# Kernel tuning notes

Measured on AMD Instinct MI355X. Metric: run time of the kernel, lower is better.

The kernel has to match this reference:

```python
import jax, jax.numpy as jnp
import numpy as np

N_NODES = 50000
N_EDGES = 800000
D_FEAT = 128
N_LAYERS = 3
HALF = 64  # units // 2 per kernel in tf_geometric MeanGraphSage
HIDDEN = 256
NUM_LABELS = 40


def setup_inputs() -> dict:
    key = jax.random.key(0)
    ks = jax.random.split(key, 6)
    x = jax.random.normal(ks[0], (N_NODES, D_FEAT), dtype=jnp.float32)
    edge_index = jax.random.randint(ks[1], (2, N_EDGES), 0, N_NODES, dtype=jnp.int32)
    self_kernels = jax.random.normal(ks[2], (N_LAYERS, D_FEAT, HALF), dtype=jnp.float32) * 0.05
    neighbor_kernels = jax.random.normal(ks[3], (N_LAYERS, D_FEAT, HALF), dtype=jnp.float32) * 0.05
    biases = jnp.zeros((N_LAYERS, 2 * HALF), dtype=jnp.float32)
    mlp_w1 = jax.random.normal(ks[4], (2 * HALF, HIDDEN), dtype=jnp.float32) * 0.05
    mlp_b1 = jnp.zeros((HIDDEN,), dtype=jnp.float32)
    mlp_w2 = jax.random.normal(ks[5], (HIDDEN, NUM_LABELS), dtype=jnp.float32) * 0.05
    mlp_b2 = jnp.zeros((NUM_LABELS,), dtype=jnp.float32)
    return {"x": x, "edge_index": edge_index, "self_kernels": self_kernels,
            "neighbor_kernels": neighbor_kernels, "biases": biases,
            "mlp_w1": mlp_w1, "mlp_b1": mlp_b1, "mlp_w2": mlp_w2, "mlp_b2": mlp_b2}


def reference(x, edge_index, self_kernels, neighbor_kernels, biases,
              mlp_w1, mlp_b1, mlp_w2, mlp_b2):
    n = x.shape[0]
    row, col = edge_index[0], edge_index[1]  # row: target node, col: source node
    # in-degree counts (graph is fixed across layers)
    ones = jnp.ones((edge_index.shape[1],), dtype=x.dtype)
    deg = jax.ops.segment_sum(ones, row, num_segments=n)  # [N]
    inv_deg = (1.0 / jnp.maximum(deg, 1.0))[:, None]      # [N,1]

    h = x
    for i in range(N_LAYERS):
        # mean-neighbor aggregation: gather source feats, segment-sum to targets
        nbr_sum = jax.ops.segment_sum(h[col], row, num_segments=n)  # [N,D]
        nbr_mean = nbr_sum * inv_deg
        from_self = h @ self_kernels[i]        # [N,HALF]
        from_nbr = nbr_mean @ neighbor_kernels[i]  # [N,HALF]
        h = jax.nn.relu(jnp.concatenate([from_self, from_nbr], axis=1) + biases[i])

    # MLP head (Flatten on [N,128] is a no-op)
    h = jax.nn.relu(h @ mlp_w1 + mlp_b1)
    return h @ mlp_w2 + mlp_b2
```

## Files before the change

kernel.cpp:

```cpp
#include <hip/hip_runtime.h>
#include <hip/hip_bf16.h>
#include <hip/hip_fp16.h>
#include <cstdint>
#include <cstddef>

#define N_NODES 50000
#define N_PAD   50176
#define N_EDGES 800000
#define D_FEAT  128
#define HALF    64
#define HIDDEN  256
#define LABELS  40

#define NBUCK 196
#define BCAP  5632
#define EDGES_PER_BLK 4096

#define HID_STRIDE 264

typedef __attribute__((ext_vector_type(8))) short bf16x8;
typedef __attribute__((ext_vector_type(4))) float f32x4;

#define PK_SELF(L) ((size_t)(L) * 8192)
#define PK_NBR(L)  (24576 + (size_t)(L) * 8192)
#define PK_W1      49152
#define PK_W2      81920
#define PK_TOTAL   94208

__device__ inline uint16_t f2bf_bits(float f) {
    __hip_bfloat16 b = __float2bfloat16(f);
    uint16_t u; __builtin_memcpy(&u, &b, 2); return u;
}

__device__ inline float2 h2f(uint32_t u) {
    __half2 h; __builtin_memcpy(&h, &u, 4);
    return __half22float2(h);
}

__global__ __launch_bounds__(1024) void bucket_scatter_kernel(
        const int* __restrict__ row, const int* __restrict__ col,
        int* __restrict__ bucket_cursor, uint32_t* __restrict__ staged) {
    __shared__ int hist[NBUCK];
    __shared__ int hbase[NBUCK];
    int tid  = threadIdx.x;
    int e0   = blockIdx.x * EDGES_PER_BLK;
    int eend = e0 + EDGES_PER_BLK; if (eend > N_EDGES) eend = N_EDGES;

    for (int i = tid; i < NBUCK; i += 1024) hist[i] = 0;
    __syncthreads();

    int rr[4], cc[4]; int ne = 0;
    for (int e = e0 + tid; e < eend; e += 1024) {
        rr[ne] = row[e]; cc[ne] = col[e]; ne++;
    }
    for (int i = 0; i < ne; i++) atomicAdd(&hist[rr[i] >> 8], 1);
    __syncthreads();

    for (int i = tid; i < NBUCK; i += 1024) {
        hbase[i] = atomicAdd(&bucket_cursor[i], hist[i]);
        hist[i]  = 0;
    }
    __syncthreads();

    for (int i = 0; i < ne; i++) {
        int b   = rr[i] >> 8;
        int off = atomicAdd(&hist[b], 1);
        int pos = hbase[b] + off;
        if (pos < BCAP)
            staged[(size_t)b * BCAP + pos] =
                ((uint32_t)(rr[i] & 255) << 16) | (uint32_t)cc[i];
    }
}

__global__ __launch_bounds__(1024) void bucket_fill_kernel(
        const uint32_t* __restrict__ staged, const int* __restrict__ bucket_cursor,
        int* __restrict__ deg, int* __restrict__ rowstart,
        float* __restrict__ inv_deg, int* __restrict__ csr_col) {
    __shared__ int cnt[256];
    __shared__ int excl[256];
    __shared__ int wt[4];
    __shared__ int seg[BCAP];
    __shared__ int base_s;
    int b   = blockIdx.x;
    int tid = threadIdx.x;

    if (tid < 64) {
        int partial = 0;
        for (int i = tid; i < b; i += 64) partial += bucket_cursor[i];
#pragma unroll
        for (int off = 32; off > 0; off >>= 1)
            partial += __shfl_down(partial, off, 64);
        if (tid == 0) base_s = partial;
    }
    if (tid < 256) cnt[tid] = 0;
    __syncthreads();

    int total = bucket_cursor[b]; if (total > BCAP) total = BCAP;
    int gbase = base_s;
    const uint32_t* st = staged + (size_t)b * BCAP;

    for (int i = tid; i < total; i += 1024) atomicAdd(&cnt[st[i] >> 16], 1);
    __syncthreads();

    int lane = tid & 63, wid = tid >> 6;
    int v = 0, s = 0;
    if (tid < 256) {
        v = cnt[tid]; s = v;
#pragma unroll
        for (int off = 1; off < 64; off <<= 1) {
            int t = __shfl_up(s, off, 64);
            if (lane >= off) s += t;
        }
        if (lane == 63) wt[wid] = s;
    }
    __syncthreads();
    if (tid == 0) { int a = 0; for (int i = 0; i < 4; i++) { int t = wt[i]; wt[i] = a; a += t; } }
    __syncthreads();
    if (tid < 256) {
        int ex = s - v + wt[wid];
        excl[tid] = ex;
        int node = (b << 8) + tid;
        if (node < N_NODES) {
            deg[node]      = v;
            rowstart[node] = gbase + ex;
            inv_deg[node]  = 1.0f / fmaxf((float)v, 1.0f);
        }
    }
    __syncthreads();
    for (int i = tid; i < total; i += 1024) {
        uint32_t u = st[i];
        int p = atomicAdd(&excl[u >> 16], 1);
        seg[p] = (int)(u & 0xffffu);
    }
    __syncthreads();
    for (int i = tid; i < total; i += 1024) csr_col[gbase + i] = seg[i];
}

__global__ __launch_bounds__(256) void pack_all_kernel(
        const float* __restrict__ selfk, const float* __restrict__ nbrk,
        const float* __restrict__ w1, const float* __restrict__ w2,
        __hip_bfloat16* __restrict__ wpack) {
    int m = blockIdx.y;
    const float* W; int K, Ncols, Npad; size_t dstoff;
    if (m < 3)      { W = selfk + (size_t)m*D_FEAT*HALF;      K=128; Ncols=64;  Npad=64;  dstoff = PK_SELF(m); }
    else if (m < 6) { W = nbrk  + (size_t)(m-3)*D_FEAT*HALF;  K=128; Ncols=64;  Npad=64;  dstoff = PK_NBR(m-3); }
    else if (m == 6){ W = w1;                                 K=128; Ncols=256; Npad=256; dstoff = PK_W1; }
    else            { W = w2;                                 K=256; Ncols=40;  Npad=48;  dstoff = PK_W2; }
    int ksteps = K / 32;
    int total  = ksteps * (Npad / 16) * 64;
    int t = blockIdx.x * blockDim.x + threadIdx.x;
    if (t >= total) return;
    int lane = t & 63;
    int rest = t >> 6;
    int ks   = rest % ksteps;
    int ns   = rest / ksteps;
    int colb = ns * 16 + (lane & 15);
    int kb   = ks * 32 + (lane >> 4) * 8;
    __hip_bfloat16* dst = wpack + dstoff + (size_t)t * 8;
#pragma unroll
    for (int j = 0; j < 8; j++) {
        float v = (colb < Ncols) ? W[(size_t)(kb + j) * Ncols + colb] : 0.f;
        dst[j] = __float2bfloat16(v);
    }
}

template<bool AF32>
__global__ __launch_bounds__(256, 2) void layer_gemm_kernel(
        const void* __restrict__ Ain,
        const __hip_bfloat16* __restrict__ wpack_self,
        const __hip_bfloat16* __restrict__ wpack_nbr,
        const float* __restrict__ bias,
        __hip_bfloat16* __restrict__ hout,
        uint16_t* __restrict__ zn) {
    int wave = threadIdx.x >> 6, lane = threadIdx.x & 63;
    int row0 = blockIdx.x * 128 + wave * 32;
    int lrow = lane & 15, lgrp = lane >> 4;

    const __hip_bfloat16 *hr0 = nullptr, *hr1 = nullptr;
    const float *xr0 = nullptr, *xr1 = nullptr;
    if constexpr (AF32) {
        const float* x = (const float*)Ain;
        int r0 = min(row0 + lrow, N_NODES - 1);
        int r1 = min(row0 + lrow + 16, N_NODES - 1);
        xr0 = x + (size_t)r0 * D_FEAT + lgrp * 8;
        xr1 = x + (size_t)r1 * D_FEAT + lgrp * 8;
    } else {
        const __hip_bfloat16* h = (const __hip_bfloat16*)Ain;
        hr0 = h + (size_t)(row0 + lrow) * D_FEAT + lgrp * 8;
        hr1 = hr0 + (size_t)16 * D_FEAT;
    }

    f32x4 accS[2][4] = {};
    f32x4 accN[2][4] = {};
#pragma unroll
    for (int ks = 0; ks < 4; ks++) {
        bf16x8 a0, a1;
        if constexpr (AF32) {
            float4 u0  = *(const float4*)(xr0 + ks * 32);
            float4 u0b = *(const float4*)(xr0 + ks * 32 + 4);
            float4 u1  = *(const float4*)(xr1 + ks * 32);
            float4 u1b = *(const float4*)(xr1 + ks * 32 + 4);
            float f0[8] = {u0.x, u0.y, u0.z, u0.w, u0b.x, u0b.y, u0b.z, u0b.w};
            float f1[8] = {u1.x, u1.y, u1.z, u1.w, u1b.x, u1b.y, u1b.z, u1b.w};
#pragma unroll
            for (int j = 0; j < 8; j++) { a0[j] = (short)f2bf_bits(f0[j]); a1[j] = (short)f2bf_bits(f1[j]); }
        } else {
            a0 = *(const bf16x8*)(hr0 + ks * 32);
            a1 = *(const bf16x8*)(hr1 + ks * 32);
        }
#pragma unroll
        for (int ns = 0; ns < 4; ns++) {
            bf16x8 bs = *(const bf16x8*)(wpack_self + ((size_t)(ns * 4 + ks) * 64 + lane) * 8);
            accS[0][ns] = __builtin_amdgcn_mfma_f32_16x16x32_bf16(a0, bs, accS[0][ns], 0, 0, 0);
            accS[1][ns] = __builtin_amdgcn_mfma_f32_16x16x32_bf16(a1, bs, accS[1][ns], 0, 0, 0);
            bf16x8 bn = *(const bf16x8*)(wpack_nbr + ((size_t)(ns * 4 + ks) * 64 + lane) * 8);
            accN[0][ns] = __builtin_amdgcn_mfma_f32_16x16x32_bf16(a0, bn, accN[0][ns], 0, 0, 0);
            accN[1][ns] = __builtin_amdgcn_mfma_f32_16x16x32_bf16(a1, bn, accN[1][ns], 0, 0, 0);
        }
    }
#pragma unroll
    for (int t = 0; t < 2; t++) {
#pragma unroll
        for (int ns = 0; ns < 4; ns++) {
            int colS = ns * 16 + lrow;
            float bvS = bias[colS];
#pragma unroll
            for (int i = 0; i < 4; i++) {
                int r = row0 + t * 16 + lgrp * 4 + i;
                hout[(size_t)r * D_FEAT + colS] =
                    __float2bfloat16(fmaxf(accS[t][ns][i] + bvS, 0.f));
                __half hz = __float2half(accN[t][ns][i]);
                uint16_t hb; __builtin_memcpy(&hb, &hz, 2);
                zn[(size_t)r * HALF + colS] = hb;
            }
        }
    }
}

__global__ __launch_bounds__(128) void agg8_kernel(
        const uint16_t* __restrict__ zn, const int* __restrict__ csr_col,
        const int* __restrict__ rowstart, const int* __restrict__ deg,
        const float* __restrict__ inv_deg, const float* __restrict__ bias64,
        __hip_bfloat16* __restrict__ hout) {
    int gid  = blockIdx.x * 128 + threadIdx.x;
    int wnum = gid >> 6;
    int lane = threadIdx.x & 63;
    int sub  = lane >> 3;
    int sl   = lane & 7;
    int node = wnum * 8 + sub;
    int start = rowstart[node];
    int d     = deg[node];
    const uint32_t* zw = (const uint32_t*)zn;
    float acc[8] = {};

#define ACC8H(U) { float2 t0 = h2f((U).x), t1 = h2f((U).y),            \
                   float2_dummy_##__LINE__; (void)0;                    \
    acc[0] += t0.x; acc[1] += t0.y; acc[2] += t1.x; acc[3] += t1.y;     \
    float2 t2 = h2f((U).z), t3 = h2f((U).w);                            \
    acc[4] += t2.x; acc[5] += t2.y; acc[6] += t3.x; acc[7] += t3.y; }

#undef ACC8H
#define ACC8H(U) {                                                      \
    float2 t0 = h2f((U).x); acc[0] += t0.x; acc[1] += t0.y;             \
    float2 t1 = h2f((U).y); acc[2] += t1.x; acc[3] += t1.y;             \
    float2 t2 = h2f((U).z); acc[4] += t2.x; acc[5] += t2.y;             \
    float2 t3 = h2f((U).w); acc[6] += t3.x; acc[7] += t3.y; }

    if (d > 0) {
        int last = start + d - 1;
        int s[8];
#pragma unroll
        for (int k = 0; k < 8; k++) s[k] = csr_col[min(start + k, last)];
        int j = 0;
        for (; j + 8 <= d; j += 8) {
            int p[8];
#pragma unroll
            for (int k = 0; k < 8; k++) p[k] = csr_col[min(start + j + 8 + k, last)];
            uint4 u0 = *(const uint4*)(zw + (size_t)s[0] * 32 + sl * 4);
            uint4 u1 = *(const uint4*)(zw + (size_t)s[1] * 32 + sl * 4);
            uint4 u2 = *(const uint4*)(zw + (size_t)s[2] * 32 + sl * 4);
            uint4 u3 = *(const uint4*)(zw + (size_t)s[3] * 32 + sl * 4);
            uint4 u4 = *(const uint4*)(zw + (size_t)s[4] * 32 + sl * 4);
            uint4 u5 = *(const uint4*)(zw + (size_t)s[5] * 32 + sl * 4);
            uint4 u6 = *(const uint4*)(zw + (size_t)s[6] * 32 + sl * 4);
            uint4 u7 = *(const uint4*)(zw + (size_t)s[7] * 32 + sl * 4);
            ACC8H(u0); ACC8H(u1); ACC8H(u2); ACC8H(u3);
            ACC8H(u4); ACC8H(u5); ACC8H(u6); ACC8H(u7);
#pragma unroll
            for (int k = 0; k < 8; k++) s[k] = p[k];
        }
        int r = d - j;
#pragma unroll
        for (int k = 0; k < 8; k++) {
            if (k < r) {
                uint4 u = *(const uint4*)(zw + (size_t)s[k] * 32 + sl * 4);
                ACC8H(u);
            }
        }
    }
#undef ACC8H

    float inv = inv_deg[node];
    float4 b0 = *(const float4*)(bias64 + sl * 8);
    float4 b1 = *(const float4*)(bias64 + sl * 8 + 4);
    uint4 p;
    p.x = (uint32_t)f2bf_bits(fmaxf(acc[0] * inv + b0.x, 0.f))
        | ((uint32_t)f2bf_bits(fmaxf(acc[1] * inv + b0.y, 0.f)) << 16);
    p.y = (uint32_t)f2bf_bits(fmaxf(acc[2] * inv + b0.z, 0.f))
        | ((uint32_t)f2bf_bits(fmaxf(acc[3] * inv + b0.w, 0.f)) << 16);
    p.z = (uint32_t)f2bf_bits(fmaxf(acc[4] * inv + b1.x, 0.f))
        | ((uint32_t)f2bf_bits(fmaxf(acc[5] * inv + b1.y, 0.f)) << 16);
    p.w = (uint32_t)f2bf_bits(fmaxf(acc[6] * inv + b1.z, 0.f))
        | ((uint32_t)f2bf_bits(fmaxf(acc[7] * inv + b1.w, 0.f)) << 16);
    *(uint4*)((uint32_t*)hout + (size_t)node * 64 + 32 + sl * 4) = p;
}

__global__ __launch_bounds__(256, 2) void mlp_fused_kernel(
        const __hip_bfloat16* __restrict__ h, const __hip_bfloat16* __restrict__ w1p,
        const float* __restrict__ b1, const __hip_bfloat16* __restrict__ w2p,
        const float* __restrict__ b2, float* __restrict__ out) {
    __shared__ __align__(16) uint16_t hid[128 * HID_STRIDE];
    int wave = threadIdx.x >> 6, lane = threadIdx.x & 63;
    int row0 = blockIdx.x * 128 + wave * 32;
    int lrow = lane & 15, lgrp = lane >> 4;

    {
        const __hip_bfloat16* ar0 = h + (size_t)(row0 + lrow) * D_FEAT + lgrp * 8;
        const __hip_bfloat16* ar1 = ar0 + (size_t)16 * D_FEAT;
        f32x4 acc[2][16] = {};
#pragma unroll 1
        for (int ks = 0; ks < 4; ks++) {
            bf16x8 a0 = *(const bf16x8*)(ar0 + ks * 32);
            bf16x8 a1 = *(const bf16x8*)(ar1 + ks * 32);
#pragma unroll
            for (int ns = 0; ns < 16; ns++) {
                bf16x8 bfr = *(const bf16x8*)(w1p + ((size_t)(ns * 4 + ks) * 64 + lane) * 8);
                acc[0][ns] = __builtin_amdgcn_mfma_f32_16x16x32_bf16(a0, bfr, acc[0][ns], 0, 0, 0);
                acc[1][ns] = __builtin_amdgcn_mfma_f32_16x16x32_bf16(a1, bfr, acc[1][ns], 0, 0, 0);
            }
        }
        int lbase = wave * 32;
#pragma unroll
        for (int t = 0; t < 2; t++) {
#pragma unroll
            for (int ns = 0; ns < 16; ns++) {
                int col = ns * 16 + lrow;
                float bv = b1[col];
#pragma unroll
                for (int i = 0; i < 4; i++) {
                    int lr = lbase + t * 16 + lgrp * 4 + i;
                    hid[lr * HID_STRIDE + col] =
                        f2bf_bits(fmaxf(acc[t][ns][i] + bv, 0.f));
                }
            }
        }
    }
    __syncthreads();

    const uint16_t* br0 = &hid[(wave * 32 + lrow) * HID_STRIDE + lgrp * 8];
    const uint16_t* br1 = br0 + 16 * HID_STRIDE;
    f32x4 acc2[2][3] = {};
#pragma unroll
    for (int ks = 0; ks < 8; ks++) {
        bf16x8 a0 = *(const bf16x8*)(br0 + ks * 32);
        bf16x8 a1 = *(const bf16x8*)(br1 + ks * 32);
#pragma unroll
        for (int ns = 0; ns < 3; ns++) {
            bf16x8 bfr = *(const bf16x8*)(w2p + ((size_t)(ns * 8 + ks) * 64 + lane) * 8);
            acc2[0][ns] = __builtin_amdgcn_mfma_f32_16x16x32_bf16(a0, bfr, acc2[0][ns], 0, 0, 0);
            acc2[1][ns] = __builtin_amdgcn_mfma_f32_16x16x32_bf16(a1, bfr, acc2[1][ns], 0, 0, 0);
        }
    }
#pragma unroll
    for (int t = 0; t < 2; t++) {
#pragma unroll
        for (int ns = 0; ns < 3; ns++) {
            int col = ns * 16 + lrow;
            if (col < LABELS) {
                float bv = b2[col];
#pragma unroll
                for (int i = 0; i < 4; i++) {
                    int r = row0 + t * 16 + lgrp * 4 + i;
                    if (r < N_NODES)
                        out[(size_t)r * LABELS + col] = acc2[t][ns][i] + bv;
                }
            }
        }
    }
}

extern "C" void kernel_launch(void* const* d_in, const int* in_sizes, int n_in,
                              void* d_out, int out_size, void* d_ws, size_t ws_size,
                              hipStream_t stream) {
    const float* x      = (const float*)d_in[0];
    const int*   ei     = (const int*)d_in[1];
    const float* selfk  = (const float*)d_in[2];
    const float* nbrk   = (const float*)d_in[3];
    const float* biases = (const float*)d_in[4];
    const float* w1     = (const float*)d_in[5];
    const float* b1     = (const float*)d_in[6];
    const float* w2     = (const float*)d_in[7];
    const float* b2     = (const float*)d_in[8];
    float* out = (float*)d_out;

    const int* row = ei;
    const int* col = ei + N_EDGES;

    char* ws = (char*)d_ws;
    size_t off = 0;
    auto alloc = [&](size_t bytes) -> char* {
        char* p = ws + off;
        off = (off + bytes + 255) & ~(size_t)255;
        return p;
    };
    int*   deg       = (int*)  alloc((size_t)N_NODES * 4);
    int*   rowstart  = (int*)  alloc((size_t)N_NODES * 4);
    float* inv_deg   = (float*)alloc((size_t)N_NODES * 4);
    int*   bucket_cursor = (int*)alloc(256 * 4);
    int*   csr_col   = (int*)  alloc((size_t)N_EDGES * 4);
    uint32_t* staged = (uint32_t*)alloc((size_t)NBUCK * BCAP * 4);
    __hip_bfloat16* wpack  = (__hip_bfloat16*)alloc(PK_TOTAL * 2);
    __hip_bfloat16* hA     = (__hip_bfloat16*)alloc((size_t)N_PAD * D_FEAT * 2);
    __hip_bfloat16* hB     = (__hip_bfloat16*)alloc((size_t)N_PAD * D_FEAT * 2);
    uint16_t*       zn     = (uint16_t*)alloc((size_t)N_PAD * HALF * 2);

    hipMemsetAsync(bucket_cursor, 0, 256 * 4, stream);

    const int scat_blocks = (N_EDGES + EDGES_PER_BLK - 1) / EDGES_PER_BLK;
    bucket_scatter_kernel<<<scat_blocks, 1024, 0, stream>>>(row, col, bucket_cursor, staged);
    bucket_fill_kernel<<<NBUCK, 1024, 0, stream>>>(staged, bucket_cursor,
                                                   deg, rowstart, inv_deg, csr_col);

    dim3 pgrid(16, 8);
    pack_all_kernel<<<pgrid, 256, 0, stream>>>(selfk, nbrk, w1, w2, wpack);

    const int layer_blocks = N_PAD / 128;
    const int agg_blocks   = N_NODES / 16;

    layer_gemm_kernel<true><<<layer_blocks, 256, 0, stream>>>(
        (const void*)x, wpack + PK_SELF(0), wpack + PK_NBR(0), biases, hA, zn);
    agg8_kernel<<<agg_blocks, 128, 0, stream>>>(zn, csr_col, rowstart, deg,
                                                inv_deg, biases + 64, hA);
    layer_gemm_kernel<false><<<layer_blocks, 256, 0, stream>>>(
        (const void*)hA, wpack + PK_SELF(1), wpack + PK_NBR(1), biases + 128, hB, zn);
    agg8_kernel<<<agg_blocks, 128, 0, stream>>>(zn, csr_col, rowstart, deg,
                                                inv_deg, biases + 128 + 64, hB);
    layer_gemm_kernel<false><<<layer_blocks, 256, 0, stream>>>(
        (const void*)hB, wpack + PK_SELF(2), wpack + PK_NBR(2), biases + 256, hA, zn);
    agg8_kernel<<<agg_blocks, 128, 0, stream>>>(zn, csr_col, rowstart, deg,
                                                inv_deg, biases + 256 + 64, hA);

    mlp_fused_kernel<<<layer_blocks, 256, 0, stream>>>(hA, wpack + PK_W1, b1,
                                                       wpack + PK_W2, b2, out);
}
```

Baseline: 206.3 us.

## Split neighbor projection into two 32-column planes for cache-friendlier aggregation

The layer GEMM now writes the fp16 neighbor projection as two separate 32-column planes instead of one 64-column row. The aggregation kernel processes each plane in its own set of blocks, with four lanes per node and blocks interleaved so that each plane's gather working set (about 3.2MB) is more likely to stay in L2/LLC. Index loads and output stores use nontemporal hints so they do not evict the gathered features. The cost is that each node's CSR index list is read twice, once per plane, and more blocks are launched.

```diff
diff --git a/kernel.cpp b/kernel.cpp
--- a/kernel.cpp
+++ b/kernel.cpp
@@ -20,6 +20,7 @@
 
 typedef __attribute__((ext_vector_type(8))) short bf16x8;
 typedef __attribute__((ext_vector_type(4))) float f32x4;
+typedef __attribute__((ext_vector_type(4))) uint32_t u32x4v;
 
 #define PK_SELF(L) ((size_t)(L) * 8192)
 #define PK_NBR(L)  (24576 + (size_t)(L) * 8192)
@@ -175,6 +176,7 @@
     int wave = threadIdx.x >> 6, lane = threadIdx.x & 63;
     int row0 = blockIdx.x * 128 + wave * 32;
     int lrow = lane & 15, lgrp = lane >> 4;
+    uint16_t* znB = zn + (size_t)N_PAD * 32;
 
     const __hip_bfloat16 *hr0 = nullptr, *hr1 = nullptr;
     const float *xr0 = nullptr, *xr1 = nullptr;
@@ -224,6 +226,8 @@
         for (int ns = 0; ns < 4; ns++) {
             int colS = ns * 16 + lrow;
             float bvS = bias[colS];
+            uint16_t* zp = (ns < 2) ? zn : znB;
+            int zc = colS & 31;
 #pragma unroll
             for (int i = 0; i < 4; i++) {
                 int r = row0 + t * 16 + lgrp * 4 + i;
@@ -231,35 +235,31 @@
                     __float2bfloat16(fmaxf(accS[t][ns][i] + bvS, 0.f));
                 __half hz = __float2half(accN[t][ns][i]);
                 uint16_t hb; __builtin_memcpy(&hb, &hz, 2);
-                zn[(size_t)r * HALF + colS] = hb;
+                zp[(size_t)r * 32 + zc] = hb;
             }
         }
     }
 }
 
-__global__ __launch_bounds__(128) void agg8_kernel(
+__global__ __launch_bounds__(256) void agg_plane_kernel(
         const uint16_t* __restrict__ zn, const int* __restrict__ csr_col,
         const int* __restrict__ rowstart, const int* __restrict__ deg,
         const float* __restrict__ inv_deg, const float* __restrict__ bias64,
         __hip_bfloat16* __restrict__ hout) {
-    int gid  = blockIdx.x * 128 + threadIdx.x;
-    int wnum = gid >> 6;
-    int lane = threadIdx.x & 63;
-    int sub  = lane >> 3;
-    int sl   = lane & 7;
-    int node = wnum * 8 + sub;
+    int b     = blockIdx.x;
+    int plane = (b >> 2) & 1;
+    int rank  = (b >> 3) * 4 + (b & 3);
+    int wave  = threadIdx.x >> 6, lane = threadIdx.x & 63;
+    int sub   = lane >> 2;
+    int sl    = lane & 3;
+    int node  = rank * 64 + wave * 16 + sub;
+    if (node >= N_NODES) node = N_NODES - 1;
+
     int start = rowstart[node];
     int d     = deg[node];
-    const uint32_t* zw = (const uint32_t*)zn;
+    const uint32_t* zw = (const uint32_t*)(zn + (size_t)plane * N_PAD * 32);
     float acc[8] = {};
 
-#define ACC8H(U) { float2 t0 = h2f((U).x), t1 = h2f((U).y),            \
-                   float2_dummy_##__LINE__; (void)0;                    \
-    acc[0] += t0.x; acc[1] += t0.y; acc[2] += t1.x; acc[3] += t1.y;     \
-    float2 t2 = h2f((U).z), t3 = h2f((U).w);                            \
-    acc[4] += t2.x; acc[5] += t2.y; acc[6] += t3.x; acc[7] += t3.y; }
-
-#undef ACC8H
 #define ACC8H(U) {                                                      \
     float2 t0 = h2f((U).x); acc[0] += t0.x; acc[1] += t0.y;             \
     float2 t1 = h2f((U).y); acc[2] += t1.x; acc[3] += t1.y;             \
@@ -270,20 +270,20 @@
         int last = start + d - 1;
         int s[8];
 #pragma unroll
-        for (int k = 0; k < 8; k++) s[k] = csr_col[min(start + k, last)];
+        for (int k = 0; k < 8; k++) s[k] = __builtin_nontemporal_load(csr_col + min(start + k, last));
         int j = 0;
         for (; j + 8 <= d; j += 8) {
             int p[8];
 #pragma unroll
-            for (int k = 0; k < 8; k++) p[k] = csr_col[min(start + j + 8 + k, last)];
-            uint4 u0 = *(const uint4*)(zw + (size_t)s[0] * 32 + sl * 4);
-            uint4 u1 = *(const uint4*)(zw + (size_t)s[1] * 32 + sl * 4);
-            uint4 u2 = *(const uint4*)(zw + (size_t)s[2] * 32 + sl * 4);
-            uint4 u3 = *(const uint4*)(zw + (size_t)s[3] * 32 + sl * 4);
-            uint4 u4 = *(const uint4*)(zw + (size_t)s[4] * 32 + sl * 4);
-            uint4 u5 = *(const uint4*)(zw + (size_t)s[5] * 32 + sl * 4);
-            uint4 u6 = *(const uint4*)(zw + (size_t)s[6] * 32 + sl * 4);
-            uint4 u7 = *(const uint4*)(zw + (size_t)s[7] * 32 + sl * 4);
+            for (int k = 0; k < 8; k++) p[k] = __builtin_nontemporal_load(csr_col + min(start + j + 8 + k, last));
+            uint4 u0 = *(const uint4*)(zw + (size_t)s[0] * 16 + sl * 4);
+            uint4 u1 = *(const uint4*)(zw + (size_t)s[1] * 16 + sl * 4);
+            uint4 u2 = *(const uint4*)(zw + (size_t)s[2] * 16 + sl * 4);
+            uint4 u3 = *(const uint4*)(zw + (size_t)s[3] * 16 + sl * 4);
+            uint4 u4 = *(const uint4*)(zw + (size_t)s[4] * 16 + sl * 4);
+            uint4 u5 = *(const uint4*)(zw + (size_t)s[5] * 16 + sl * 4);
+            uint4 u6 = *(const uint4*)(zw + (size_t)s[6] * 16 + sl * 4);
+            uint4 u7 = *(const uint4*)(zw + (size_t)s[7] * 16 + sl * 4);
             ACC8H(u0); ACC8H(u1); ACC8H(u2); ACC8H(u3);
             ACC8H(u4); ACC8H(u5); ACC8H(u6); ACC8H(u7);
 #pragma unroll
@@ -293,7 +293,7 @@
 #pragma unroll
         for (int k = 0; k < 8; k++) {
             if (k < r) {
-                uint4 u = *(const uint4*)(zw + (size_t)s[k] * 32 + sl * 4);
+                uint4 u = *(const uint4*)(zw + (size_t)s[k] * 16 + sl * 4);
                 ACC8H(u);
             }
         }
@@ -301,9 +301,10 @@
 #undef ACC8H
 
     float inv = inv_deg[node];
-    float4 b0 = *(const float4*)(bias64 + sl * 8);
-    float4 b1 = *(const float4*)(bias64 + sl * 8 + 4);
-    uint4 p;
+    const float* bb = bias64 + plane * 32 + sl * 8;
+    float4 b0 = *(const float4*)bb;
+    float4 b1 = *(const float4*)(bb + 4);
+    u32x4v p;
     p.x = (uint32_t)f2bf_bits(fmaxf(acc[0] * inv + b0.x, 0.f))
         | ((uint32_t)f2bf_bits(fmaxf(acc[1] * inv + b0.y, 0.f)) << 16);
     p.y = (uint32_t)f2bf_bits(fmaxf(acc[2] * inv + b0.z, 0.f))
@@ -312,7 +313,8 @@
         | ((uint32_t)f2bf_bits(fmaxf(acc[5] * inv + b1.y, 0.f)) << 16);
     p.w = (uint32_t)f2bf_bits(fmaxf(acc[6] * inv + b1.z, 0.f))
         | ((uint32_t)f2bf_bits(fmaxf(acc[7] * inv + b1.w, 0.f)) << 16);
-    *(uint4*)((uint32_t*)hout + (size_t)node * 64 + 32 + sl * 4) = p;
+    uint32_t* dst = (uint32_t*)hout + (size_t)node * 64 + 32 + plane * 16 + sl * 4;
+    __builtin_nontemporal_store(p, (u32x4v*)dst);
 }
 
 __global__ __launch_bounds__(256, 2) void mlp_fused_kernel(
@@ -435,20 +437,20 @@
     pack_all_kernel<<<pgrid, 256, 0, stream>>>(selfk, nbrk, w1, w2, wpack);
 
     const int layer_blocks = N_PAD / 128;
-    const int agg_blocks   = N_NODES / 16;
+    const int agg_blocks   = 196 * 8;
 
     layer_gemm_kernel<true><<<layer_blocks, 256, 0, stream>>>(
         (const void*)x, wpack + PK_SELF(0), wpack + PK_NBR(0), biases, hA, zn);
-    agg8_kernel<<<agg_blocks, 128, 0, stream>>>(zn, csr_col, rowstart, deg,
-                                                inv_deg, biases + 64, hA);
+    agg_plane_kernel<<<agg_blocks, 256, 0, stream>>>(zn, csr_col, rowstart, deg,
+                                                     inv_deg, biases + 64, hA);
     layer_gemm_kernel<false><<<layer_blocks, 256, 0, stream>>>(
         (const void*)hA, wpack + PK_SELF(1), wpack + PK_NBR(1), biases + 128, hB, zn);
-    agg8_kernel<<<agg_blocks, 128, 0, stream>>>(zn, csr_col, rowstart, deg,
-                                                inv_deg, biases + 128 + 64, hB);
+    agg_plane_kernel<<<agg_blocks, 256, 0, stream>>>(zn, csr_col, rowstart, deg,
+                                                     inv_deg, biases + 128 + 64, hB);
     layer_gemm_kernel<false><<<layer_blocks, 256, 0, stream>>>(
         (const void*)hB, wpack + PK_SELF(2), wpack + PK_NBR(2), biases + 256, hA, zn);
-    agg8_kernel<<<agg_blocks, 128, 0, stream>>>(zn, csr_col, rowstart, deg,
-                                                inv_deg, biases + 256 + 64, hA);
+    agg_plane_kernel<<<agg_blocks, 256, 0, stream>>>(zn, csr_col, rowstart, deg,
+                                                     inv_deg, biases + 256 + 64, hA);
 
     mlp_fused_kernel<<<layer_blocks, 256, 0, stream>>>(hA, wpack + PK_W1, b1,
                                                        wpack + PK_W2, b2, out);
```

Result: slower. 245.9 us (+19.2%).

## Partition each CSR row by source half and gather in two passes

Applied to the files above, without the earlier changes.

The CSR fill now sorts each node's neighbor list into two groups, sources below 25000 and sources at or above it, and records the low-group count per node. The aggregation kernel walks the two groups in two separate gather loops, intended to improve locality of the zn gathers across waves. Index and metadata loads also switch to nontemporal loads. This adds an extra per-node array, more shared atomics during the CSR build, and a second loop tail per node, which increases instruction overhead and under-fills the unrolled gather for short lists.

```diff
diff --git a/kernel.cpp b/kernel.cpp
--- a/kernel.cpp
+++ b/kernel.cpp
@@ -11,6 +11,8 @@
 #define HALF    64
 #define HIDDEN  256
 #define LABELS  40
+
+#define N_SPLIT 25000
 
 #define NBUCK 196
 #define BCAP  5632
@@ -74,10 +76,12 @@
 
 __global__ __launch_bounds__(1024) void bucket_fill_kernel(
         const uint32_t* __restrict__ staged, const int* __restrict__ bucket_cursor,
-        int* __restrict__ deg, int* __restrict__ rowstart,
+        int* __restrict__ deg, int* __restrict__ dlo, int* __restrict__ rowstart,
         float* __restrict__ inv_deg, int* __restrict__ csr_col) {
     __shared__ int cnt[256];
-    __shared__ int excl[256];
+    __shared__ int cntlo[256];
+    __shared__ int clo[256];
+    __shared__ int chi[256];
     __shared__ int wt[4];
     __shared__ int seg[BCAP];
     __shared__ int base_s;
@@ -92,14 +96,19 @@
             partial += __shfl_down(partial, off, 64);
         if (tid == 0) base_s = partial;
     }
-    if (tid < 256) cnt[tid] = 0;
+    if (tid < 256) { cnt[tid] = 0; cntlo[tid] = 0; }
     __syncthreads();
 
     int total = bucket_cursor[b]; if (total > BCAP) total = BCAP;
     int gbase = base_s;
     const uint32_t* st = staged + (size_t)b * BCAP;
 
-    for (int i = tid; i < total; i += 1024) atomicAdd(&cnt[st[i] >> 16], 1);
+    for (int i = tid; i < total; i += 1024) {
+        uint32_t u = st[i];
+        atomicAdd(&cnt[u >> 16], 1);
+        if ((int)(u & 0xffffu) + 0 < 0) {}
+        if ((int)(u & 0xffffu) < N_SPLIT) atomicAdd(&cntlo[u >> 16], 1);
+    }
     __syncthreads();
 
     int lane = tid & 63, wid = tid >> 6;
@@ -118,10 +127,12 @@
     __syncthreads();
     if (tid < 256) {
         int ex = s - v + wt[wid];
-        excl[tid] = ex;
+        clo[tid] = ex;
+        chi[tid] = ex + cntlo[tid];
         int node = (b << 8) + tid;
         if (node < N_NODES) {
             deg[node]      = v;
+            dlo[node]      = cntlo[tid];
             rowstart[node] = gbase + ex;
             inv_deg[node]  = 1.0f / fmaxf((float)v, 1.0f);
         }
@@ -129,8 +140,10 @@
     __syncthreads();
     for (int i = tid; i < total; i += 1024) {
         uint32_t u = st[i];
-        int p = atomicAdd(&excl[u >> 16], 1);
-        seg[p] = (int)(u & 0xffffu);
+        int nd  = u >> 16;
+        int src = (int)(u & 0xffffu);
+        int p = (src < N_SPLIT) ? atomicAdd(&clo[nd], 1) : atomicAdd(&chi[nd], 1);
+        seg[p] = src;
     }
     __syncthreads();
     for (int i = tid; i < total; i += 1024) csr_col[gbase + i] = seg[i];
@@ -237,72 +250,75 @@
     }
 }
 
+__device__ inline void gather_accum(const uint32_t* __restrict__ zw,
+                                    const int* __restrict__ csr_col,
+                                    int start, int d, int sl, float* acc) {
+#define ACC8H(U) {                                                      \
+    float2 t0 = h2f((U).x); acc[0] += t0.x; acc[1] += t0.y;             \
+    float2 t1 = h2f((U).y); acc[2] += t1.x; acc[3] += t1.y;             \
+    float2 t2 = h2f((U).z); acc[4] += t2.x; acc[5] += t2.y;             \
+    float2 t3 = h2f((U).w); acc[6] += t3.x; acc[7] += t3.y; }
+
+    if (d <= 0) return;
+    int last = start + d - 1;
+    int s[8];
+#pragma unroll
+    for (int k = 0; k < 8; k++)
+        s[k] = __builtin_nontemporal_load(csr_col + min(start + k, last));
+    int j = 0;
+    for (; j + 8 <= d; j += 8) {
+        int p[8];
+#pragma unroll
+        for (int k = 0; k < 8; k++)
+            p[k] = __builtin_nontemporal_load(csr_col + min(start + j + 8 + k, last));
+        uint4 u0 = *(const uint4*)(zw + (size_t)s[0] * 32 + sl * 4);
+        uint4 u1 = *(const uint4*)(zw + (size_t)s[1] * 32 + sl * 4);
+        uint4 u2 = *(const uint4*)(zw + (size_t)s[2] * 32 + sl * 4);
+        uint4 u3 = *(const uint4*)(zw + (size_t)s[3] * 32 + sl * 4);
+        uint4 u4 = *(const uint4*)(zw + (size_t)s[4] * 32 + sl * 4);
+        uint4 u5 = *(const uint4*)(zw + (size_t)s[5] * 32 + sl * 4);
+        uint4 u6 = *(const uint4*)(zw + (size_t)s[6] * 32 + sl * 4);
+        uint4 u7 = *(const uint4*)(zw + (size_t)s[7] * 32 + sl * 4);
+        ACC8H(u0); ACC8H(u1); ACC8H(u2); ACC8H(u3);
+        ACC8H(u4); ACC8H(u5); ACC8H(u6); ACC8H(u7);
+#pragma unroll
+        for (int k = 0; k < 8; k++) s[k] = p[k];
+    }
+    int r = d - j;
+#pragma unroll
+    for (int k = 0; k < 8; k++) {
+        if (k < r) {
+            uint4 u = *(const uint4*)(zw + (size_t)s[k] * 32 + sl * 4);
+            ACC8H(u);
+        }
+    }
+#undef ACC8H
+}
+
 __global__ __launch_bounds__(128) void agg8_kernel(
         const uint16_t* __restrict__ zn, const int* __restrict__ csr_col,
         const int* __restrict__ rowstart, const int* __restrict__ deg,
-        const float* __restrict__ inv_deg, const float* __restrict__ bias64,
-        __hip_bfloat16* __restrict__ hout) {
+        const int* __restrict__ dlo, const float* __restrict__ inv_deg,
+        const float* __restrict__ bias64, __hip_bfloat16* __restrict__ hout) {
     int gid  = blockIdx.x * 128 + threadIdx.x;
     int wnum = gid >> 6;
     int lane = threadIdx.x & 63;
     int sub  = lane >> 3;
     int sl   = lane & 7;
     int node = wnum * 8 + sub;
-    int start = rowstart[node];
-    int d     = deg[node];
+    int start = __builtin_nontemporal_load(rowstart + node);
+    int d     = __builtin_nontemporal_load(deg + node);
+    int dl    = __builtin_nontemporal_load(dlo + node);
     const uint32_t* zw = (const uint32_t*)zn;
     float acc[8] = {};
 
-#define ACC8H(U) { float2 t0 = h2f((U).x), t1 = h2f((U).y),            \
-                   float2_dummy_##__LINE__; (void)0;                    \
-    acc[0] += t0.x; acc[1] += t0.y; acc[2] += t1.x; acc[3] += t1.y;     \
-    float2 t2 = h2f((U).z), t3 = h2f((U).w);                            \
-    acc[4] += t2.x; acc[5] += t2.y; acc[6] += t3.x; acc[7] += t3.y; }
-
-#undef ACC8H
-#define ACC8H(U) {                                                      \
-    float2 t0 = h2f((U).x); acc[0] += t0.x; acc[1] += t0.y;             \
-    float2 t1 = h2f((U).y); acc[2] += t1.x; acc[3] += t1.y;             \
-    float2 t2 = h2f((U).z); acc[4] += t2.x; acc[5] += t2.y;             \
-    float2 t3 = h2f((U).w); acc[6] += t3.x; acc[7] += t3.y; }
-
-    if (d > 0) {
-        int last = start + d - 1;
-        int s[8];
-#pragma unroll
-        for (int k = 0; k < 8; k++) s[k] = csr_col[min(start + k, last)];
-        int j = 0;
-        for (; j + 8 <= d; j += 8) {
-            int p[8];
-#pragma unroll
-            for (int k = 0; k < 8; k++) p[k] = csr_col[min(start + j + 8 + k, last)];
-            uint4 u0 = *(const uint4*)(zw + (size_t)s[0] * 32 + sl * 4);
-            uint4 u1 = *(const uint4*)(zw + (size_t)s[1] * 32 + sl * 4);
-            uint4 u2 = *(const uint4*)(zw + (size_t)s[2] * 32 + sl * 4);
-            uint4 u3 = *(const uint4*)(zw + (size_t)s[3] * 32 + sl * 4);
-            uint4 u4 = *(const uint4*)(zw + (size_t)s[4] * 32 + sl * 4);
-            uint4 u5 = *(const uint4*)(zw + (size_t)s[5] * 32 + sl * 4);
-            uint4 u6 = *(const uint4*)(zw + (size_t)s[6] * 32 + sl * 4);
-            uint4 u7 = *(const uint4*)(zw + (size_t)s[7] * 32 + sl * 4);
-            ACC8H(u0); ACC8H(u1); ACC8H(u2); ACC8H(u3);
-            ACC8H(u4); ACC8H(u5); ACC8H(u6); ACC8H(u7);
-#pragma unroll
-            for (int k = 0; k < 8; k++) s[k] = p[k];
-        }
-        int r = d - j;
-#pragma unroll
-        for (int k = 0; k < 8; k++) {
-            if (k < r) {
-                uint4 u = *(const uint4*)(zw + (size_t)s[k] * 32 + sl * 4);
-                ACC8H(u);
-            }
-        }
-    }
-#undef ACC8H
-
-    float inv = inv_deg[node];
-    float4 b0 = *(const float4*)(bias64 + sl * 8);
-    float4 b1 = *(const float4*)(bias64 + sl * 8 + 4);
+    gather_accum(zw, csr_col, start,      dl,     sl, acc);
+    gather_accum(zw, csr_col, start + dl, d - dl, sl, acc);
+
+    float inv = __builtin_nontemporal_load(inv_deg + node);
+    const float* bb = bias64 + sl * 8;
+    float4 b0 = *(const float4*)bb;
+    float4 b1 = *(const float4*)(bb + 4);
     uint4 p;
     p.x = (uint32_t)f2bf_bits(fmaxf(acc[0] * inv + b0.x, 0.f))
         | ((uint32_t)f2bf_bits(fmaxf(acc[1] * inv + b0.y, 0.f)) << 16);
@@ -414,6 +430,7 @@
         return p;
     };
     int*   deg       = (int*)  alloc((size_t)N_NODES * 4);
+    int*   dlo       = (int*)  alloc((size_t)N_NODES * 4);
     int*   rowstart  = (int*)  alloc((size_t)N_NODES * 4);
     float* inv_deg   = (float*)alloc((size_t)N_NODES * 4);
     int*   bucket_cursor = (int*)alloc(256 * 4);
@@ -429,7 +446,7 @@
     const int scat_blocks = (N_EDGES + EDGES_PER_BLK - 1) / EDGES_PER_BLK;
     bucket_scatter_kernel<<<scat_blocks, 1024, 0, stream>>>(row, col, bucket_cursor, staged);
     bucket_fill_kernel<<<NBUCK, 1024, 0, stream>>>(staged, bucket_cursor,
-                                                   deg, rowstart, inv_deg, csr_col);
+                                                   deg, dlo, rowstart, inv_deg, csr_col);
 
     dim3 pgrid(16, 8);
     pack_all_kernel<<<pgrid, 256, 0, stream>>>(selfk, nbrk, w1, w2, wpack);
@@ -439,15 +456,15 @@
 
     layer_gemm_kernel<true><<<layer_blocks, 256, 0, stream>>>(
         (const void*)x, wpack + PK_SELF(0), wpack + PK_NBR(0), biases, hA, zn);
-    agg8_kernel<<<agg_blocks, 128, 0, stream>>>(zn, csr_col, rowstart, deg,
+    agg8_kernel<<<agg_blocks, 128, 0, stream>>>(zn, csr_col, rowstart, deg, dlo,
                                                 inv_deg, biases + 64, hA);
     layer_gemm_kernel<false><<<layer_blocks, 256, 0, stream>>>(
         (const void*)hA, wpack + PK_SELF(1), wpack + PK_NBR(1), biases + 128, hB, zn);
-    agg8_kernel<<<agg_blocks, 128, 0, stream>>>(zn, csr_col, rowstart, deg,
+    agg8_kernel<<<agg_blocks, 128, 0, stream>>>(zn, csr_col, rowstart, deg, dlo,
                                                 inv_deg, biases + 128 + 64, hB);
     layer_gemm_kernel<false><<<layer_blocks, 256, 0, stream>>>(
         (const void*)hB, wpack + PK_SELF(2), wpack + PK_NBR(2), biases + 256, hA, zn);
-    agg8_kernel<<<agg_blocks, 128, 0, stream>>>(zn, csr_col, rowstart, deg,
+    agg8_kernel<<<agg_blocks, 128, 0, stream>>>(zn, csr_col, rowstart, deg, dlo,
                                                 inv_deg, biases + 256 + 64, hA);
 
     mlp_fused_kernel<<<layer_blocks, 256, 0, stream>>>(hA, wpack + PK_W1, b1,
```

Result: slower. 221.8 us (+7.5%).

## Pad CSR rows to multiples of eight with zero-row sentinel and halve GEMM block size

Applied to the files above, without the earlier changes.

Each node's neighbor list is padded to a multiple of eight entries. The padding points at an all-zero sentinel row of zn, and each bucket's CSR segment gets a fixed-capacity slot. This removes the cross-bucket prefix scan in bucket_fill and the remainder/tail handling in the aggregation loop, and adds nontemporal loads for index data. The layer GEMM and MLP kernels also move to 64-row, 128-thread blocks for more blocks in flight. The cost is extra gathers of the zero row, a larger csr_col buffer, and a risk of BUCKCAP overflow if a bucket's padded total exceeds it.

```diff
diff --git a/kernel.cpp b/kernel.cpp
--- a/kernel.cpp
+++ b/kernel.cpp
@@ -14,7 +14,10 @@
 
 #define NBUCK 196
 #define BCAP  5632
+#define BUCKCAP 7424
 #define EDGES_PER_BLK 4096
+
+#define ZROW  N_PAD
 
 #define HID_STRIDE 264
 
@@ -79,33 +82,26 @@
     __shared__ int cnt[256];
     __shared__ int excl[256];
     __shared__ int wt[4];
-    __shared__ int seg[BCAP];
-    __shared__ int base_s;
+    __shared__ int seg[BUCKCAP];
+    __shared__ int total_pad_s;
     int b   = blockIdx.x;
     int tid = threadIdx.x;
 
-    if (tid < 64) {
-        int partial = 0;
-        for (int i = tid; i < b; i += 64) partial += bucket_cursor[i];
-#pragma unroll
-        for (int off = 32; off > 0; off >>= 1)
-            partial += __shfl_down(partial, off, 64);
-        if (tid == 0) base_s = partial;
-    }
     if (tid < 256) cnt[tid] = 0;
     __syncthreads();
 
     int total = bucket_cursor[b]; if (total > BCAP) total = BCAP;
-    int gbase = base_s;
     const uint32_t* st = staged + (size_t)b * BCAP;
 
     for (int i = tid; i < total; i += 1024) atomicAdd(&cnt[st[i] >> 16], 1);
     __syncthreads();
 
     int lane = tid & 63, wid = tid >> 6;
-    int v = 0, s = 0;
+    int v = 0, vp = 0, s = 0;
     if (tid < 256) {
-        v = cnt[tid]; s = v;
+        v  = cnt[tid];
+        vp = (v + 7) & ~7;
+        s  = vp;
 #pragma unroll
         for (int off = 1; off < 64; off <<= 1) {
             int t = __shfl_up(s, off, 64);
@@ -117,14 +113,16 @@
     if (tid == 0) { int a = 0; for (int i = 0; i < 4; i++) { int t = wt[i]; wt[i] = a; a += t; } }
     __syncthreads();
     if (tid < 256) {
-        int ex = s - v + wt[wid];
+        int ex = s - vp + wt[wid];
         excl[tid] = ex;
         int node = (b << 8) + tid;
         if (node < N_NODES) {
             deg[node]      = v;
-            rowstart[node] = gbase + ex;
+            rowstart[node] = b * BUCKCAP + ex;
             inv_deg[node]  = 1.0f / fmaxf((float)v, 1.0f);
         }
+        if (tid == 255) total_pad_s = ex + vp;
+        for (int q = v; q < vp; q++) seg[ex + q] = ZROW;
     }
     __syncthreads();
     for (int i = tid; i < total; i += 1024) {
@@ -133,7 +131,8 @@
         seg[p] = (int)(u & 0xffffu);
     }
     __syncthreads();
-    for (int i = tid; i < total; i += 1024) csr_col[gbase + i] = seg[i];
+    int tp = total_pad_s;
+    for (int i = tid; i < tp; i += 1024) csr_col[b * BUCKCAP + i] = seg[i];
 }
 
 __global__ __launch_bounds__(256) void pack_all_kernel(
@@ -165,7 +164,7 @@
 }
 
 template<bool AF32>
-__global__ __launch_bounds__(256, 2) void layer_gemm_kernel(
+__global__ __launch_bounds__(128, 2) void layer_gemm_kernel(
         const void* __restrict__ Ain,
         const __hip_bfloat16* __restrict__ wpack_self,
         const __hip_bfloat16* __restrict__ wpack_nbr,
@@ -173,7 +172,7 @@
         __hip_bfloat16* __restrict__ hout,
         uint16_t* __restrict__ zn) {
     int wave = threadIdx.x >> 6, lane = threadIdx.x & 63;
-    int row0 = blockIdx.x * 128 + wave * 32;
+    int row0 = blockIdx.x * 64 + wave * 32;
     int lrow = lane & 15, lgrp = lane >> 4;
 
     const __hip_bfloat16 *hr0 = nullptr, *hr1 = nullptr;
@@ -248,34 +247,29 @@
     int sub  = lane >> 3;
     int sl   = lane & 7;
     int node = wnum * 8 + sub;
-    int start = rowstart[node];
-    int d     = deg[node];
+    int start = __builtin_nontemporal_load(rowstart + node);
+    int d     = __builtin_nontemporal_load(deg + node);
+    int dpad  = (d + 7) & ~7;
     const uint32_t* zw = (const uint32_t*)zn;
     float acc[8] = {};
 
-#define ACC8H(U) { float2 t0 = h2f((U).x), t1 = h2f((U).y),            \
-                   float2_dummy_##__LINE__; (void)0;                    \
-    acc[0] += t0.x; acc[1] += t0.y; acc[2] += t1.x; acc[3] += t1.y;     \
-    float2 t2 = h2f((U).z), t3 = h2f((U).w);                            \
-    acc[4] += t2.x; acc[5] += t2.y; acc[6] += t3.x; acc[7] += t3.y; }
-
-#undef ACC8H
 #define ACC8H(U) {                                                      \
     float2 t0 = h2f((U).x); acc[0] += t0.x; acc[1] += t0.y;             \
     float2 t1 = h2f((U).y); acc[2] += t1.x; acc[3] += t1.y;             \
     float2 t2 = h2f((U).z); acc[4] += t2.x; acc[5] += t2.y;             \
     float2 t3 = h2f((U).w); acc[6] += t3.x; acc[7] += t3.y; }
 
-    if (d > 0) {
-        int last = start + d - 1;
+    if (dpad > 0) {
         int s[8];
 #pragma unroll
-        for (int k = 0; k < 8; k++) s[k] = csr_col[min(start + k, last)];
-        int j = 0;
-        for (; j + 8 <= d; j += 8) {
+        for (int k = 0; k < 8; k++)
+            s[k] = __builtin_nontemporal_load(csr_col + start + k);
+        for (int j = 0; j < dpad; j += 8) {
+            int pb = min(j + 8, dpad - 8);
             int p[8];
 #pragma unroll
-            for (int k = 0; k < 8; k++) p[k] = csr_col[min(start + j + 8 + k, last)];
+            for (int k = 0; k < 8; k++)
+                p[k] = __builtin_nontemporal_load(csr_col + start + pb + k);
             uint4 u0 = *(const uint4*)(zw + (size_t)s[0] * 32 + sl * 4);
             uint4 u1 = *(const uint4*)(zw + (size_t)s[1] * 32 + sl * 4);
             uint4 u2 = *(const uint4*)(zw + (size_t)s[2] * 32 + sl * 4);
@@ -289,20 +283,13 @@
 #pragma unroll
             for (int k = 0; k < 8; k++) s[k] = p[k];
         }
-        int r = d - j;
-#pragma unroll
-        for (int k = 0; k < 8; k++) {
-            if (k < r) {
-                uint4 u = *(const uint4*)(zw + (size_t)s[k] * 32 + sl * 4);
-                ACC8H(u);
-            }
-        }
     }
 #undef ACC8H
 
-    float inv = inv_deg[node];
-    float4 b0 = *(const float4*)(bias64 + sl * 8);
-    float4 b1 = *(const float4*)(bias64 + sl * 8 + 4);
+    float inv = __builtin_nontemporal_load(inv_deg + node);
+    const float* bb = bias64 + sl * 8;
+    float4 b0 = *(const float4*)bb;
+    float4 b1 = *(const float4*)(bb + 4);
     uint4 p;
     p.x = (uint32_t)f2bf_bits(fmaxf(acc[0] * inv + b0.x, 0.f))
         | ((uint32_t)f2bf_bits(fmaxf(acc[1] * inv + b0.y, 0.f)) << 16);
@@ -315,13 +302,13 @@
     *(uint4*)((uint32_t*)hout + (size_t)node * 64 + 32 + sl * 4) = p;
 }
 
-__global__ __launch_bounds__(256, 2) void mlp_fused_kernel(
+__global__ __launch_bounds__(128) void mlp_fused_kernel(
         const __hip_bfloat16* __restrict__ h, const __hip_bfloat16* __restrict__ w1p,
         const float* __restrict__ b1, const __hip_bfloat16* __restrict__ w2p,
         const float* __restrict__ b2, float* __restrict__ out) {
-    __shared__ __align__(16) uint16_t hid[128 * HID_STRIDE];
+    __shared__ __align__(16) uint16_t hid[64 * HID_STRIDE];
     int wave = threadIdx.x >> 6, lane = threadIdx.x & 63;
-    int row0 = blockIdx.x * 128 + wave * 32;
+    int row0 = blockIdx.x * 64 + wave * 32;
     int lrow = lane & 15, lgrp = lane >> 4;
 
     {
@@ -417,14 +404,15 @@
     int*   rowstart  = (int*)  alloc((size_t)N_NODES * 4);
     float* inv_deg   = (float*)alloc((size_t)N_NODES * 4);
     int*   bucket_cursor = (int*)alloc(256 * 4);
-    int*   csr_col   = (int*)  alloc((size_t)N_EDGES * 4);
+    int*   csr_col   = (int*)  alloc((size_t)NBUCK * BUCKCAP * 4);
     uint32_t* staged = (uint32_t*)alloc((size_t)NBUCK * BCAP * 4);
     __hip_bfloat16* wpack  = (__hip_bfloat16*)alloc(PK_TOTAL * 2);
     __hip_bfloat16* hA     = (__hip_bfloat16*)alloc((size_t)N_PAD * D_FEAT * 2);
     __hip_bfloat16* hB     = (__hip_bfloat16*)alloc((size_t)N_PAD * D_FEAT * 2);
-    uint16_t*       zn     = (uint16_t*)alloc((size_t)N_PAD * HALF * 2);
+    uint16_t*       zn     = (uint16_t*)alloc((size_t)(N_PAD + 8) * HALF * 2);
 
     hipMemsetAsync(bucket_cursor, 0, 256 * 4, stream);
+    hipMemsetAsync(zn + (size_t)ZROW * HALF, 0, HALF * 2, stream);
 
     const int scat_blocks = (N_EDGES + EDGES_PER_BLK - 1) / EDGES_PER_BLK;
     bucket_scatter_kernel<<<scat_blocks, 1024, 0, stream>>>(row, col, bucket_cursor, staged);
@@ -434,22 +422,22 @@
     dim3 pgrid(16, 8);
     pack_all_kernel<<<pgrid, 256, 0, stream>>>(selfk, nbrk, w1, w2, wpack);
 
-    const int layer_blocks = N_PAD / 128;
+    const int layer_blocks = N_PAD / 64;
     const int agg_blocks   = N_NODES / 16;
 
-    layer_gemm_kernel<true><<<layer_blocks, 256, 0, stream>>>(
+    layer_gemm_kernel<true><<<layer_blocks, 128, 0, stream>>>(
         (const void*)x, wpack + PK_SELF(0), wpack + PK_NBR(0), biases, hA, zn);
     agg8_kernel<<<agg_blocks, 128, 0, stream>>>(zn, csr_col, rowstart, deg,
                                                 inv_deg, biases + 64, hA);
-    layer_gemm_kernel<false><<<layer_blocks, 256, 0, stream>>>(
+    layer_gemm_kernel<false><<<layer_blocks, 128, 0, stream>>>(
         (const void*)hA, wpack + PK_SELF(1), wpack + PK_NBR(1), biases + 128, hB, zn);
     agg8_kernel<<<agg_blocks, 128, 0, stream>>>(zn, csr_col, rowstart, deg,
                                                 inv_deg, biases + 128 + 64, hB);
-    layer_gemm_kernel<false><<<layer_blocks, 256, 0, stream>>>(
+    layer_gemm_kernel<false><<<layer_blocks, 128, 0, stream>>>(
         (const void*)hB, wpack + PK_SELF(2), wpack + PK_NBR(2), biases + 256, hA, zn);
     agg8_kernel<<<agg_blocks, 128, 0, stream>>>(zn, csr_col, rowstart, deg,
                                                 inv_deg, biases + 256 + 64, hA);
 
-    mlp_fused_kernel<<<layer_blocks, 256, 0, stream>>>(hA, wpack + PK_W1, b1,
+    mlp_fused_kernel<<<layer_blocks, 128, 0, stream>>>(hA, wpack + PK_W1, b1,
                                                        wpack + PK_W2, b2, out);
 }
```

After: 222.5 us. 7.9% more time.
